# Performance work log

Measured on AMD Instinct MI355X. Metric: run time of the kernel, lower is better.

The kernel has to match this reference:

```python
import jax, jax.numpy as jnp
import numpy as np

B, T, N_EMBD = 4, 2048, 1024
NUM_EXPERTS, TOP_K = 8, 2
N_CITIES = 4
LIN = N_EMBD + 32 + N_EMBD // 4 + N_EMBD // 4 + N_EMBD // 8 + N_EMBD // 8  # 1824


def setup_inputs() -> dict:
    key = jax.random.key(0)
    ks = jax.random.split(key, 12)
    s = 0.02  # init std as in _init_weights
    return {
        "x": jax.random.normal(ks[0], (B, T, N_EMBD), jnp.float32),
        "delta_t_info": jax.random.normal(ks[1], (B, T, N_EMBD // 4), jnp.float32),
        "delta_dis_info": jax.random.normal(ks[2], (B, T, N_EMBD // 4), jnp.float32),
        "delta_rg_info": jax.random.normal(ks[3], (B, T, N_EMBD // 8), jnp.float32),
        "delta_entropy_info": jax.random.normal(ks[4], (B, T, N_EMBD // 8), jnp.float32),
        "city_embeddings": jax.random.normal(ks[5], (N_CITIES, 32), jnp.float32),
        "Wg": jax.random.normal(ks[6], (LIN, NUM_EXPERTS), jnp.float32) * s,
        "bg": jnp.zeros((NUM_EXPERTS,), jnp.float32),
        "W1": jax.random.normal(ks[7], (NUM_EXPERTS, N_EMBD, 4 * N_EMBD), jnp.float32) * s,
        "b1": jnp.zeros((NUM_EXPERTS, 4 * N_EMBD), jnp.float32),
        "W2": jax.random.normal(ks[8], (NUM_EXPERTS, 4 * N_EMBD, N_EMBD), jnp.float32) * s,
        "b2": jnp.zeros((NUM_EXPERTS, N_EMBD), jnp.float32),
        "city_index": 1,
    }


def _moe(x, dt, dd, drg, de, city_embeddings, Wg, bg, W1, b1, W2, b2, city_index):
    b, t, _ = x.shape
    city = jnp.broadcast_to(city_embeddings[city_index], (b, t, 32))
    feats = jnp.concatenate([x, city, dt, dd, drg, de], axis=-1)  # [B,T,LIN]
    logits = jnp.einsum("btl,le->bte", feats, Wg) + bg            # eval mode: no noise
    gate1 = jax.nn.softmax(logits, axis=-1)
    _, topi = jax.lax.top_k(logits, TOP_K)                        # [B,T,k]
    # mask of top-k experts per token; scatter(-inf elsewhere) + softmax
    mask = jax.nn.one_hot(topi, NUM_EXPERTS, dtype=jnp.float32).sum(axis=-2) > 0
    sparse_logits = jnp.where(mask, logits, -jnp.inf)
    gates = jax.nn.softmax(sparse_logits, axis=-1)                # zeros outside top-k
    out = jnp.zeros_like(x)
    for e in range(NUM_EXPERTS):  # fixed small expert set
        h = jax.nn.gelu(jnp.einsum("btc,ch->bth", x, W1[e]) + b1[e], approximate=True)
        y = jnp.einsum("bth,hc->btc", h, W2[e]) + b2[e]
        out = out + gates[..., e:e + 1] * y  # gate is exactly 0 for non-topk tokens
    return out, gate1


def reference(x, delta_t_info, delta_dis_info, delta_rg_info, delta_entropy_info,
              city_embeddings, Wg, bg, W1, b1, W2, b2, city_index):
    return _moe(x, delta_t_info, delta_dis_info, delta_rg_info, delta_entropy_info,
                city_embeddings, Wg, bg, W1, b1, W2, b2, city_index)
```

## Files before the change

### kernel.cpp

```cpp
#include <hip/hip_runtime.h>
#include <hip/hip_bf16.h>
#include <stdint.h>

#define NTOK 8192
#define DEMB 1024
#define HDIM 4096
#define NEXP 8
#define LINF 1824
#define MAXPAD 17280

typedef __attribute__((ext_vector_type(8))) __bf16 bf16x8;
typedef __attribute__((ext_vector_type(4))) __bf16 bf16x4v;
typedef __attribute__((ext_vector_type(4))) float f32x4;

__device__ __forceinline__ void gload_lds16(const void* g, void* l) {
  __builtin_amdgcn_global_load_lds(
      (const __attribute__((address_space(1))) void*)g,
      (__attribute__((address_space(3))) void*)l, 16, 0, 0);
}

__device__ __forceinline__ float dot4(float4 a, float4 b) {
  return a.x*b.x + a.y*b.y + a.z*b.z + a.w*b.w;
}

__global__ void __launch_bounds__(256) k_logits(
    const float* __restrict__ x, const float* __restrict__ dt,
    const float* __restrict__ dd, const float* __restrict__ drg,
    const float* __restrict__ de, const float* __restrict__ city,
    const float* __restrict__ Wg, const float* __restrict__ bg,
    const int* __restrict__ city_index,
    float* __restrict__ gate1, int* __restrict__ top_i, float2* __restrict__ top_g)
{
  __shared__ float WgT[NEXP * LINF];
  const int tid = threadIdx.x;
  const float4* Wg4 = (const float4*)Wg;
  for (int i = tid; i < LINF * NEXP / 4; i += 256) {
    float4 v = Wg4[i];
    int e0 = (i & 1) * 4, f = i >> 1;
    WgT[(e0+0)*LINF + f] = v.x; WgT[(e0+1)*LINF + f] = v.y;
    WgT[(e0+2)*LINF + f] = v.z; WgT[(e0+3)*LINF + f] = v.w;
  }
  __syncthreads();

  const int wave = tid >> 6, lane = tid & 63;
  const int ci = city_index[0];
  const float4* city4 = (const float4*)(city + ci*32);
  const float4 z4 = {0.f, 0.f, 0.f, 0.f};

  #pragma unroll
  for (int k = 0; k < 4; ++k) {
    const int t = blockIdx.x*16 + wave*4 + k;
    const float4* x4 = (const float4*)x + (size_t)t*256;
    float4 xv0 = x4[lane], xv1 = x4[64+lane], xv2 = x4[128+lane], xv3 = x4[192+lane];
    float4 cv = (lane < 8) ? city4[lane] : z4;
    float4 tv = ((const float4*)dt)[(size_t)t*64 + lane];
    float4 dv = ((const float4*)dd)[(size_t)t*64 + lane];
    float4 rv = z4, ev = z4;
    if (lane < 32) {
      rv = ((const float4*)drg)[(size_t)t*32 + lane];
      ev = ((const float4*)de )[(size_t)t*32 + lane];
    }
    float a[8];
    const int l8 = lane & 7, l32 = lane & 31;
    #pragma unroll
    for (int e = 0; e < 8; ++e) {
      const float4* W = (const float4*)(WgT + e*LINF);
      float s = dot4(xv0, W[lane]) + dot4(xv1, W[64+lane])
              + dot4(xv2, W[128+lane]) + dot4(xv3, W[192+lane]);
      s += dot4(cv, W[256 + l8]);
      s += dot4(tv, W[264 + lane]) + dot4(dv, W[328 + lane]);
      s += dot4(rv, W[392 + l32]) + dot4(ev, W[424 + l32]);
      a[e] = s;
    }
    #pragma unroll
    for (int off = 32; off > 0; off >>= 1)
      #pragma unroll
      for (int e = 0; e < 8; ++e) a[e] += __shfl_xor(a[e], off);

    float lg[8];
    #pragma unroll
    for (int e = 0; e < 8; ++e) lg[e] = a[e] + bg[e];
    float mx = lg[0];
    #pragma unroll
    for (int e = 1; e < 8; ++e) mx = fmaxf(mx, lg[e]);
    float ex[8]; float s = 0.f;
    #pragma unroll
    for (int e = 0; e < 8; ++e) { ex[e] = expf(lg[e] - mx); s += ex[e]; }
    int i1 = 0; float l1 = lg[0];
    #pragma unroll
    for (int e = 1; e < 8; ++e) if (lg[e] > l1) { l1 = lg[e]; i1 = e; }
    int i2 = -1; float l2 = -1e30f;
    #pragma unroll
    for (int e = 0; e < 8; ++e) if (e != i1 && lg[e] > l2) { l2 = lg[e]; i2 = e; }
    float e2 = expf(l2 - l1);

    if (lane == 0) {
      float inv = 1.f / s;
      float4 o0 = { ex[0]*inv, ex[1]*inv, ex[2]*inv, ex[3]*inv };
      float4 o1 = { ex[4]*inv, ex[5]*inv, ex[6]*inv, ex[7]*inv };
      float4* gp = (float4*)(gate1 + (size_t)t*8);
      gp[0] = o0; gp[1] = o1;
      top_i[t] = i1 | (i2 << 4);
      float2 g = { 1.f / (1.f + e2), e2 / (1.f + e2) };
      top_g[t] = g;
    }
  }
}

__global__ void __launch_bounds__(256) k_build(
    const int* __restrict__ top_i, const float2* __restrict__ top_g,
    int* __restrict__ counts, int* __restrict__ ex_tok, float* __restrict__ ex_gate,
    int2* __restrict__ ppos)
{
  __shared__ int lcnt[8], lbase[8];
  const int tid = threadIdx.x;
  if (tid < 8) lcnt[tid] = 0;
  __syncthreads();
  const int t = blockIdx.x*256 + tid;
  const int ti = top_i[t];
  const int i1 = ti & 15, i2 = ti >> 4;
  const float2 g = top_g[t];
  int p1 = atomicAdd(&lcnt[i1], 1);
  int p2 = atomicAdd(&lcnt[i2], 1);
  __syncthreads();
  if (tid < 8) lbase[tid] = atomicAdd(&counts[tid], lcnt[tid]);
  __syncthreads();
  int s1 = lbase[i1] + p1; ex_tok[i1*NTOK+s1] = t; ex_gate[i1*NTOK+s1] = g.x;
  int s2 = lbase[i2] + p2; ex_tok[i2*NTOK+s2] = t; ex_gate[i2*NTOK+s2] = g.y;
  int2 pp = { i1 | (s1 << 3), i2 | (s2 << 3) };
  ppos[t] = pp;
}

__global__ void k_finalize(const int* __restrict__ counts, int* __restrict__ seg) {
  if (threadIdx.x == 0 && blockIdx.x == 0) {
    int s = 0;
    for (int e = 0; e < 8; ++e) { seg[e] = s; s += (counts[e] + 127) & ~127; }
    seg[8] = s;
  }
}

__global__ void __launch_bounds__(256) k_conv_x(
    const float4* __restrict__ x, bf16x4v* __restrict__ xb, int n4)
{
  int step = gridDim.x * blockDim.x;
  for (int i = blockIdx.x*blockDim.x + threadIdx.x; i < n4; i += step) {
    float4 v = x[i];
    bf16x4v o;
    o[0] = (__bf16)v.x; o[1] = (__bf16)v.y; o[2] = (__bf16)v.z; o[3] = (__bf16)v.w;
    xb[i] = o;
  }
}

template<int RDIM, int CDIM>
__global__ void __launch_bounds__(256) k_tconv(
    const float* __restrict__ W, __bf16* __restrict__ WT)
{
  const int e  = blockIdx.z;
  const int c0 = blockIdx.x * 64, r0 = blockIdx.y * 64;
  __shared__ float tb[64 * 65];
  const float* src = W  + (size_t)e * RDIM * CDIM + (size_t)r0 * CDIM + c0;
  __bf16*      dst = WT + (size_t)e * RDIM * CDIM + (size_t)c0 * RDIM + r0;
  const int tx = threadIdx.x & 15, ty = threadIdx.x >> 4;
  #pragma unroll
  for (int i = 0; i < 4; ++i) {
    int r = ty + i*16;
    float4 v = *(const float4*)(src + (size_t)r*CDIM + tx*4);
    tb[(tx*4+0)*65 + r] = v.x; tb[(tx*4+1)*65 + r] = v.y;
    tb[(tx*4+2)*65 + r] = v.z; tb[(tx*4+3)*65 + r] = v.w;
  }
  __syncthreads();
  const int seg = threadIdx.x & 7, dr8 = threadIdx.x >> 3;
  #pragma unroll
  for (int i = 0; i < 2; ++i) {
    int d = dr8 + i*32;
    const float* row = tb + d*65 + seg*8;
    bf16x8 o;
    #pragma unroll
    for (int j = 0; j < 8; ++j) o[j] = (__bf16)row[j];
    *(bf16x8*)(dst + (size_t)d*RDIM + seg*8) = o;
  }
}

template<int KDIM, int NDIM, bool G1>
__global__ void __launch_bounds__(512, 2) k_moe_gemm(
    const __bf16* __restrict__ Abase, const __bf16* __restrict__ WT,
    const float* __restrict__ bias,
    const int* __restrict__ seg, const int* __restrict__ counts,
    const int* __restrict__ ex_tok,
    int chunk0, __bf16* __restrict__ dstbuf)
{
  constexpr int NT = KDIM / 64;
  constexpr int BUFB = 49152;

  const int nx = gridDim.x, ny = gridDim.y;
  const int nwg = nx * ny;
  int flat = blockIdx.x + nx * blockIdx.y;
  {
    int q = nwg >> 3, r = nwg & 7;
    int xcd = flat & 7, idx = flat >> 3;
    flat = (xcd < r ? xcd * (q + 1) : r * (q + 1) + (xcd - r) * q) + idx;
  }
  int bx, by;
  if (G1) { bx = flat % nx; by = flat / nx; }
  else    { by = flat % ny; bx = flat / ny; }

  const int segtot = seg[8];
  const int row0 = chunk0 + bx * 128;
  if (row0 >= segtot) return;
  int e = 0;
  #pragma unroll
  for (int qq = 1; qq < 8; ++qq) if (row0 >= seg[qq]) e = qq;
  const int cnt  = counts[e];
  const int sege = seg[e];
  const int n0 = by * 256;

  __shared__ __align__(16) char smem[3 * BUFB];

  const int tid = threadIdx.x;
  const int wid = tid >> 6, lane = tid & 63;
  const int wm = wid >> 2, wn = wid & 3;
  const int l15 = lane & 15, l4 = lane >> 4;
  const __bf16* Bsrc = WT + (size_t)e * NDIM * KDIM;

  const __bf16* asrc[2]; const __bf16* bsrc[4];
  #pragma unroll
  for (int i = 0; i < 2; ++i) {
    int g = i*512 + tid;
    int rr = g >> 3;
    int kb = (g & 7) ^ (rr & 7);
    int arow;
    if (G1) {
      int lr = row0 + rr - sege;
      arow = (lr < cnt) ? ex_tok[e*NTOK + lr] : 0;
    } else {
      arow = row0 + rr - chunk0;
    }
    asrc[i] = Abase + (size_t)arow * KDIM + kb*8;
  }
  #pragma unroll
  for (int i = 0; i < 4; ++i) {
    int g = i*512 + tid;
    int rr = g >> 3;
    int kb = (g & 7) ^ (rr & 7);
    bsrc[i] = Bsrc + (size_t)(n0 + rr) * KDIM + kb*8;
  }

  int aoff[2][4], boff[2][4];
  #pragma unroll
  for (int kk = 0; kk < 2; ++kk) {
    const int kblk = kk*4 + l4;
    const int xo = (kblk ^ (l15 & 7)) * 16;
    #pragma unroll
    for (int m = 0; m < 4; ++m)
      aoff[kk][m] = (wm*64 + m*16 + l15)*128 + xo;
    #pragma unroll
    for (int n = 0; n < 4; ++n)
      boff[kk][n] = 16384 + (wn*64 + n*16 + l15)*128 + xo;
  }

  float bv[4];
  #pragma unroll
  for (int n = 0; n < 4; ++n)
    bv[n] = bias[(size_t)e*NDIM + n0 + wn*64 + n*16 + l15];

  auto STAGE = [&](int t, int b) {
    char* base = smem + b*BUFB;
    #pragma unroll
    for (int i = 0; i < 2; ++i)
      gload_lds16(asrc[i] + t*64, base + (i*512 + tid)*16);
    #pragma unroll
    for (int i = 0; i < 4; ++i)
      gload_lds16(bsrc[i] + t*64, base + 16384 + (i*512 + tid)*16);
  };

  f32x4 acc[4][4] = {};

  STAGE(0, 0);
  STAGE(1, 1);
  asm volatile("s_waitcnt vmcnt(6)" ::: "memory");
  __builtin_amdgcn_s_barrier();
  __builtin_amdgcn_sched_barrier(0);

  int cur = 0;
  for (int t = 0; t < NT; ++t) {
    const char* cb = smem + cur*BUFB;
    int b2 = cur + 2; if (b2 >= 3) b2 -= 3;
    char* sb = smem + b2*BUFB;
    const bool dost = (t + 2 < NT);

    {
      bf16x8 af[4], bfv[4];
      #pragma unroll
      for (int m = 0; m < 4; ++m) af[m]  = *(const bf16x8*)(cb + aoff[0][m]);
      #pragma unroll
      for (int n = 0; n < 4; ++n) bfv[n] = *(const bf16x8*)(cb + boff[0][n]);
      if (dost) {
        gload_lds16(asrc[0] + (t+2)*64, sb + (0*512 + tid)*16);
        gload_lds16(asrc[1] + (t+2)*64, sb + (1*512 + tid)*16);
        gload_lds16(bsrc[0] + (t+2)*64, sb + 16384 + (0*512 + tid)*16);
      }
      __builtin_amdgcn_sched_barrier(0);
      __builtin_amdgcn_s_barrier();
      __builtin_amdgcn_s_setprio(1);
      #pragma unroll
      for (int m = 0; m < 4; ++m)
        #pragma unroll
        for (int n = 0; n < 4; ++n)
          acc[m][n] = __builtin_amdgcn_mfma_f32_16x16x32_bf16(af[m], bfv[n], acc[m][n], 0, 0, 0);
      __builtin_amdgcn_s_setprio(0);
      __builtin_amdgcn_sched_barrier(0);
      __builtin_amdgcn_s_barrier();
    }
    {
      bf16x8 af[4], bfv[4];
      #pragma unroll
      for (int m = 0; m < 4; ++m) af[m]  = *(const bf16x8*)(cb + aoff[1][m]);
      #pragma unroll
      for (int n = 0; n < 4; ++n) bfv[n] = *(const bf16x8*)(cb + boff[1][n]);
      if (dost) {
        gload_lds16(bsrc[1] + (t+2)*64, sb + 16384 + (1*512 + tid)*16);
        gload_lds16(bsrc[2] + (t+2)*64, sb + 16384 + (2*512 + tid)*16);
        gload_lds16(bsrc[3] + (t+2)*64, sb + 16384 + (3*512 + tid)*16);
      }
      __builtin_amdgcn_sched_barrier(0);
      __builtin_amdgcn_s_barrier();
      __builtin_amdgcn_s_setprio(1);
      #pragma unroll
      for (int m = 0; m < 4; ++m)
        #pragma unroll
        for (int n = 0; n < 4; ++n)
          acc[m][n] = __builtin_amdgcn_mfma_f32_16x16x32_bf16(af[m], bfv[n], acc[m][n], 0, 0, 0);
      __builtin_amdgcn_s_setprio(0);
      __builtin_amdgcn_sched_barrier(0);
      asm volatile("s_waitcnt lgkmcnt(0)" ::: "memory");
      if (dost) asm volatile("s_waitcnt vmcnt(6)" ::: "memory");
      else      asm volatile("s_waitcnt vmcnt(0)" ::: "memory");
      __builtin_amdgcn_s_barrier();
      __builtin_amdgcn_sched_barrier(0);
    }
    cur = (cur == 2) ? 0 : cur + 1;
  }

  __bf16* Cl = (__bf16*)smem;
  #pragma unroll
  for (int n = 0; n < 4; ++n) {
    #pragma unroll
    for (int m = 0; m < 4; ++m) {
      #pragma unroll
      for (int r2 = 0; r2 < 4; ++r2) {
        float v = acc[m][n][r2] + bv[n];
        if (G1) {
          float z = 2.302208f * (v + 0.044715f * v * v * v);
          v = v / (1.f + exp2f(-z));
        }
        Cl[(wm*64 + m*16 + l4*4 + r2)*256 + wn*64 + n*16 + l15] = (__bf16)v;
      }
    }
  }
  __syncthreads();
  const int drow0 = G1 ? (row0 - chunk0) : row0;
  #pragma unroll
  for (int it = 0; it < 8; ++it) {
    int idx2 = it*512 + tid;
    int rr = idx2 >> 5, c8 = (idx2 & 31) * 8;
    *(bf16x8*)(dstbuf + (size_t)(drow0 + rr)*NDIM + n0 + c8) =
        *(const bf16x8*)(Cl + rr*256 + c8);
  }
}

__global__ void __launch_bounds__(256) k_combine(
    const __bf16* __restrict__ pbuf, const int2* __restrict__ ppos,
    const float2* __restrict__ top_g, const int* __restrict__ seg,
    float* __restrict__ out)
{
  const int t = blockIdx.x;
  const int tid = threadIdx.x;
  const int2 pp = ppos[t];
  const float2 g = top_g[t];
  const int e1 = pp.x & 7, i1 = pp.x >> 3;
  const int e2 = pp.y & 7, i2 = pp.y >> 3;
  const __bf16* r1 = pbuf + (size_t)(seg[e1] + i1) * DEMB;
  const __bf16* r2 = pbuf + (size_t)(seg[e2] + i2) * DEMB;
  float* orow = out + (size_t)t * DEMB;
  const int c = tid * 4;
  bf16x4v a = *(const bf16x4v*)(r1 + c);
  bf16x4v b = *(const bf16x4v*)(r2 + c);
  float4 o;
  o.x = g.x*(float)a[0] + g.y*(float)b[0];
  o.y = g.x*(float)a[1] + g.y*(float)b[1];
  o.z = g.x*(float)a[2] + g.y*(float)b[2];
  o.w = g.x*(float)a[3] + g.y*(float)b[3];
  *(float4*)(orow + c) = o;
}

extern "C" void kernel_launch(void* const* d_in, const int* in_sizes, int n_in,
                              void* d_out, int out_size, void* d_ws, size_t ws_size,
                              hipStream_t stream)
{
  const float* x   = (const float*)d_in[0];
  const float* dt  = (const float*)d_in[1];
  const float* dd  = (const float*)d_in[2];
  const float* drg = (const float*)d_in[3];
  const float* de  = (const float*)d_in[4];
  const float* city= (const float*)d_in[5];
  const float* Wg  = (const float*)d_in[6];
  const float* bg  = (const float*)d_in[7];
  const float* W1  = (const float*)d_in[8];
  const float* b1  = (const float*)d_in[9];
  const float* W2  = (const float*)d_in[10];
  const float* b2  = (const float*)d_in[11];
  const int* city_index = (const int*)d_in[12];

  float* out   = (float*)d_out;
  float* gate1 = out + (size_t)NTOK * DEMB;

  char* p = (char*)d_ws;
  int*    counts  = (int*)p;      p += 256;
  int*    seg     = (int*)p;      p += 256;
  int*    top_i   = (int*)p;      p += (size_t)NTOK*4;
  float2* top_g   = (float2*)p;   p += (size_t)NTOK*8;
  int2*   ppos    = (int2*)p;     p += (size_t)NTOK*8;
  int*    ex_tok  = (int*)p;      p += (size_t)NTOK*NEXP*4;
  float*  ex_gate = (float*)p;    p += (size_t)NTOK*NEXP*4;
  __bf16* xb      = (__bf16*)p;   p += (size_t)NTOK*DEMB*2;
  __bf16* W1T     = (__bf16*)p;   p += (size_t)NEXP*DEMB*HDIM*2;
  __bf16* W2T     = (__bf16*)p;   p += (size_t)NEXP*DEMB*HDIM*2;
  __bf16* pbuf    = (__bf16*)p;   p += (size_t)MAXPAD*DEMB*2;
  __bf16* hbuf    = (__bf16*)p;

  size_t fixed = (size_t)(p - (char*)d_ws);
  int CH = MAXPAD;
  while (CH > 0 && fixed + (size_t)CH * HDIM * 2 > ws_size) CH -= 256;
  if (CH <= 0) return;
  int nch = (MAXPAD + CH - 1) / CH;

  (void)hipMemsetAsync(counts, 0, 64, stream);

  k_conv_x<<<2048, 256, 0, stream>>>((const float4*)x, (bf16x4v*)xb, NTOK*DEMB/4);
  k_tconv<DEMB, HDIM><<<dim3(HDIM/64, DEMB/64, NEXP), 256, 0, stream>>>(W1, W1T);
  k_tconv<HDIM, DEMB><<<dim3(DEMB/64, HDIM/64, NEXP), 256, 0, stream>>>(W2, W2T);

  k_logits<<<NTOK/16, 256, 0, stream>>>(x, dt, dd, drg, de, city, Wg, bg,
                                        city_index, gate1, top_i, top_g);
  k_build<<<NTOK/256, 256, 0, stream>>>(top_i, top_g, counts, ex_tok, ex_gate, ppos);
  k_finalize<<<1, 64, 0, stream>>>(counts, seg);

  for (int c = 0; c < nch; ++c) {
    k_moe_gemm<DEMB, HDIM, true><<<dim3(CH/128, HDIM/256), 512, 0, stream>>>(
        xb, W1T, b1, seg, counts, ex_tok, c*CH, hbuf);
    k_moe_gemm<HDIM, DEMB, false><<<dim3(CH/128, DEMB/256), 512, 0, stream>>>(
        hbuf, W2T, b2, seg, counts, ex_tok, c*CH, pbuf);
  }
  k_combine<<<NTOK, 256, 0, stream>>>(pbuf, ppos, top_g, seg, out);
}
```

Before: 549.2 us.

## Use 256x256 GEMM tiles with quadrant pipelining and split-K for second GEMM

The expert GEMM tile grows from 128x256 to 256x256 per workgroup. The k-loop becomes a double-buffered four-quadrant schedule that interleaves LDS reads, async global-to-LDS loads and MFMA blocks. Expert segments are now padded to 256 rows to fit the larger tile. The down-projection GEMM is split along K into two halves, each written to its own partial buffer, and the combine kernel sums both partials and adds b2. This is meant to raise arithmetic intensity and cut LDS/global traffic per FLOP, at the cost of more padding rows, an extra partial buffer with more combine reads, and heavier register pressure from 32 accumulators per thread.

```diff
diff --git a/kernel.cpp b/kernel.cpp
--- a/kernel.cpp
+++ b/kernel.cpp
@@ -7,7 +7,7 @@
 #define HDIM 4096
 #define NEXP 8
 #define LINF 1824
-#define MAXPAD 17280
+#define MAXPAD 18432
 
 typedef __attribute__((ext_vector_type(8))) __bf16 bf16x8;
 typedef __attribute__((ext_vector_type(4))) __bf16 bf16x4v;
@@ -134,7 +134,7 @@
 __global__ void k_finalize(const int* __restrict__ counts, int* __restrict__ seg) {
   if (threadIdx.x == 0 && blockIdx.x == 0) {
     int s = 0;
-    for (int e = 0; e < 8; ++e) { seg[e] = s; s += (counts[e] + 127) & ~127; }
+    for (int e = 0; e < 8; ++e) { seg[e] = s; s += (counts[e] + 255) & ~255; }
     seg[8] = s;
   }
 }
@@ -169,20 +169,20 @@
     tb[(tx*4+2)*65 + r] = v.z; tb[(tx*4+3)*65 + r] = v.w;
   }
   __syncthreads();
-  const int seg = threadIdx.x & 7, dr8 = threadIdx.x >> 3;
+  const int sg = threadIdx.x & 7, dr8 = threadIdx.x >> 3;
   #pragma unroll
   for (int i = 0; i < 2; ++i) {
     int d = dr8 + i*32;
-    const float* row = tb + d*65 + seg*8;
+    const float* row = tb + d*65 + sg*8;
     bf16x8 o;
     #pragma unroll
     for (int j = 0; j < 8; ++j) o[j] = (__bf16)row[j];
-    *(bf16x8*)(dst + (size_t)d*RDIM + seg*8) = o;
-  }
-}
-
-template<int KDIM, int NDIM, bool G1>
-__global__ void __launch_bounds__(512, 2) k_moe_gemm(
+    *(bf16x8*)(dst + (size_t)d*RDIM + sg*8) = o;
+  }
+}
+
+template<int KDIM, int KFULL, int NDIM, bool G1>
+__global__ void __launch_bounds__(512, 2) k_moe_gemm8(
     const __bf16* __restrict__ Abase, const __bf16* __restrict__ WT,
     const float* __restrict__ bias,
     const int* __restrict__ seg, const int* __restrict__ counts,
@@ -190,180 +190,214 @@
     int chunk0, __bf16* __restrict__ dstbuf)
 {
   constexpr int NT = KDIM / 64;
-  constexpr int BUFB = 49152;
-
-  const int nx = gridDim.x, ny = gridDim.y;
-  const int nwg = nx * ny;
-  int flat = blockIdx.x + nx * blockIdx.y;
-  {
-    int q = nwg >> 3, r = nwg & 7;
-    int xcd = flat & 7, idx = flat >> 3;
-    flat = (xcd < r ? xcd * (q + 1) : r * (q + 1) + (xcd - r) * q) + idx;
-  }
-  int bx, by;
-  if (G1) { bx = flat % nx; by = flat / nx; }
-  else    { by = flat % ny; bx = flat / ny; }
+  const int nx = gridDim.x, ny = gridDim.y, nz = gridDim.z;
+  const int total = nx * ny * nz;
+  int flat;
+  if (G1) flat = blockIdx.x + nx * blockIdx.y;
+  else    flat = blockIdx.y + ny * (blockIdx.x + nx * blockIdx.z);
+  { int q = total >> 3, r = total & 7; int xcd = flat & 7, idx = flat >> 3;
+    flat = (xcd < r ? xcd*(q+1) : r*(q+1) + (xcd-r)*q) + idx; }
+  int bx, by, bz;
+  if (G1) { bx = flat % nx; by = flat / nx; bz = 0; }
+  else    { by = flat % ny; int f2 = flat / ny; bx = f2 % nx; bz = f2 / nx; }
 
   const int segtot = seg[8];
-  const int row0 = chunk0 + bx * 128;
+  const int row0 = chunk0 + bx * 256;
   if (row0 >= segtot) return;
   int e = 0;
   #pragma unroll
   for (int qq = 1; qq < 8; ++qq) if (row0 >= seg[qq]) e = qq;
-  const int cnt  = counts[e];
-  const int sege = seg[e];
+  const int cnt = counts[e], sege = seg[e];
   const int n0 = by * 256;
-
-  __shared__ __align__(16) char smem[3 * BUFB];
+  const int kbase = bz * KDIM;
+
+  __shared__ __align__(16) char smem[131072];
 
   const int tid = threadIdx.x;
   const int wid = tid >> 6, lane = tid & 63;
   const int wm = wid >> 2, wn = wid & 3;
   const int l15 = lane & 15, l4 = lane >> 4;
-  const __bf16* Bsrc = WT + (size_t)e * NDIM * KDIM;
-
-  const __bf16* asrc[2]; const __bf16* bsrc[4];
-  #pragma unroll
-  for (int i = 0; i < 2; ++i) {
-    int g = i*512 + tid;
-    int rr = g >> 3;
-    int kb = (g & 7) ^ (rr & 7);
-    int arow;
-    if (G1) {
-      int lr = row0 + rr - sege;
-      arow = (lr < cnt) ? ex_tok[e*NTOK + lr] : 0;
-    } else {
-      arow = row0 + rr - chunk0;
-    }
-    asrc[i] = Abase + (size_t)arow * KDIM + kb*8;
-  }
-  #pragma unroll
-  for (int i = 0; i < 4; ++i) {
-    int g = i*512 + tid;
-    int rr = g >> 3;
-    int kb = (g & 7) ^ (rr & 7);
-    bsrc[i] = Bsrc + (size_t)(n0 + rr) * KDIM + kb*8;
-  }
-
-  int aoff[2][4], boff[2][4];
-  #pragma unroll
-  for (int kk = 0; kk < 2; ++kk) {
-    const int kblk = kk*4 + l4;
-    const int xo = (kblk ^ (l15 & 7)) * 16;
-    #pragma unroll
-    for (int m = 0; m < 4; ++m)
-      aoff[kk][m] = (wm*64 + m*16 + l15)*128 + xo;
-    #pragma unroll
-    for (int n = 0; n < 4; ++n)
-      boff[kk][n] = 16384 + (wn*64 + n*16 + l15)*128 + xo;
-  }
+  const __bf16* Bsrc = WT + (size_t)e * NDIM * KFULL;
 
   float bv[4];
-  #pragma unroll
-  for (int n = 0; n < 4; ++n)
-    bv[n] = bias[(size_t)e*NDIM + n0 + wn*64 + n*16 + l15];
-
-  auto STAGE = [&](int t, int b) {
-    char* base = smem + b*BUFB;
-    #pragma unroll
-    for (int i = 0; i < 2; ++i)
-      gload_lds16(asrc[i] + t*64, base + (i*512 + tid)*16);
-    #pragma unroll
-    for (int i = 0; i < 4; ++i)
-      gload_lds16(bsrc[i] + t*64, base + 16384 + (i*512 + tid)*16);
+  if (G1) {
+    #pragma unroll
+    for (int N = 0; N < 4; ++N)
+      bv[N] = bias[(size_t)e*NDIM + n0 + wn*64 + N*16 + l15];
+    asm volatile("" :: "v"(bv[0]), "v"(bv[1]), "v"(bv[2]), "v"(bv[3]));
+  }
+
+  const __bf16* sp[4][2];
+  #pragma unroll
+  for (int j = 0; j < 2; ++j) {
+    int g = j*512 + tid;
+    int sl = g >> 3;
+    int kb = (g & 7) ^ (sl & 7);
+    #pragma unroll
+    for (int mh = 0; mh < 2; ++mh) {
+      int wms = (sl >> 6) & 1, rs = sl & 63;
+      int R = wms*128 + mh*64 + rs;
+      int arow;
+      if (G1) { int lr = row0 + R - sege; arow = (lr < cnt) ? ex_tok[e*NTOK + lr] : 0; }
+      else    { arow = row0 + R - chunk0; }
+      sp[mh][j] = Abase + (size_t)arow * KFULL + kbase + kb*8;
+    }
+    #pragma unroll
+    for (int nh = 0; nh < 2; ++nh) {
+      int wns = (sl >> 5) & 3, rs = sl & 31;
+      int C = wns*64 + nh*32 + rs;
+      sp[2+nh][j] = Bsrc + (size_t)(n0 + C) * KFULL + kbase + kb*8;
+    }
+  }
+
+  int xo[2];
+  #pragma unroll
+  for (int kk = 0; kk < 2; ++kk) xo[kk] = (((kk*4 + l4) ^ (l15 & 7)) * 16);
+  int arb[4], brb[2];
+  #pragma unroll
+  for (int m = 0; m < 4; ++m) arb[m] = (wm*64 + m*16 + l15) * 128;
+  #pragma unroll
+  for (int n = 0; n < 2; ++n) brb[n] = 32768 + (wn*32 + n*16 + l15) * 128;
+
+  auto ISSUE = [&](int h, int tt) {
+    char* b = smem + (tt & 1) * 65536 + h * 16384;
+    gload_lds16(sp[h][0] + tt*64, b + tid*16);
+    gload_lds16(sp[h][1] + tt*64, b + 8192 + tid*16);
   };
 
-  f32x4 acc[4][4] = {};
-
-  STAGE(0, 0);
-  STAGE(1, 1);
-  asm volatile("s_waitcnt vmcnt(6)" ::: "memory");
+  f32x4 acc[8][4] = {};
+
+  ISSUE(0,0); ISSUE(2,0); ISSUE(3,0); ISSUE(1,0); ISSUE(0,1);
+  asm volatile("s_waitcnt vmcnt(2)" ::: "memory");
   __builtin_amdgcn_s_barrier();
   __builtin_amdgcn_sched_barrier(0);
 
-  int cur = 0;
   for (int t = 0; t < NT; ++t) {
-    const char* cb = smem + cur*BUFB;
-    int b2 = cur + 2; if (b2 >= 3) b2 -= 3;
-    char* sb = smem + b2*BUFB;
-    const bool dost = (t + 2 < NT);
-
-    {
-      bf16x8 af[4], bfv[4];
-      #pragma unroll
-      for (int m = 0; m < 4; ++m) af[m]  = *(const bf16x8*)(cb + aoff[0][m]);
-      #pragma unroll
-      for (int n = 0; n < 4; ++n) bfv[n] = *(const bf16x8*)(cb + boff[0][n]);
-      if (dost) {
-        gload_lds16(asrc[0] + (t+2)*64, sb + (0*512 + tid)*16);
-        gload_lds16(asrc[1] + (t+2)*64, sb + (1*512 + tid)*16);
-        gload_lds16(bsrc[0] + (t+2)*64, sb + 16384 + (0*512 + tid)*16);
-      }
-      __builtin_amdgcn_sched_barrier(0);
-      __builtin_amdgcn_s_barrier();
-      __builtin_amdgcn_s_setprio(1);
-      #pragma unroll
-      for (int m = 0; m < 4; ++m)
+    const char* cb = smem + (t & 1) * 65536;
+    const bool last = (t == NT - 1);
+    bf16x8 af[4][2], bfr[2][2][2];
+
+    #pragma unroll
+    for (int m = 0; m < 4; ++m)
+      #pragma unroll
+      for (int kk = 0; kk < 2; ++kk)
+        af[m][kk] = *(const bf16x8*)(cb + arb[m] + xo[kk]);
+    #pragma unroll
+    for (int n = 0; n < 2; ++n)
+      #pragma unroll
+      for (int kk = 0; kk < 2; ++kk)
+        bfr[0][n][kk] = *(const bf16x8*)(cb + brb[n] + xo[kk]);
+    if (!last) ISSUE(2, t+1);
+    __builtin_amdgcn_sched_barrier(0);
+    __builtin_amdgcn_s_barrier();
+    __builtin_amdgcn_sched_barrier(0);
+    __builtin_amdgcn_s_setprio(1);
+    #pragma unroll
+    for (int m = 0; m < 4; ++m)
+      #pragma unroll
+      for (int n = 0; n < 2; ++n)
         #pragma unroll
-        for (int n = 0; n < 4; ++n)
-          acc[m][n] = __builtin_amdgcn_mfma_f32_16x16x32_bf16(af[m], bfv[n], acc[m][n], 0, 0, 0);
-      __builtin_amdgcn_s_setprio(0);
-      __builtin_amdgcn_sched_barrier(0);
-      __builtin_amdgcn_s_barrier();
-    }
-    {
-      bf16x8 af[4], bfv[4];
-      #pragma unroll
-      for (int m = 0; m < 4; ++m) af[m]  = *(const bf16x8*)(cb + aoff[1][m]);
-      #pragma unroll
-      for (int n = 0; n < 4; ++n) bfv[n] = *(const bf16x8*)(cb + boff[1][n]);
-      if (dost) {
-        gload_lds16(bsrc[1] + (t+2)*64, sb + 16384 + (1*512 + tid)*16);
-        gload_lds16(bsrc[2] + (t+2)*64, sb + 16384 + (2*512 + tid)*16);
-        gload_lds16(bsrc[3] + (t+2)*64, sb + 16384 + (3*512 + tid)*16);
-      }
-      __builtin_amdgcn_sched_barrier(0);
-      __builtin_amdgcn_s_barrier();
-      __builtin_amdgcn_s_setprio(1);
-      #pragma unroll
-      for (int m = 0; m < 4; ++m)
+        for (int kk = 0; kk < 2; ++kk)
+          acc[m][n] = __builtin_amdgcn_mfma_f32_16x16x32_bf16(af[m][kk], bfr[0][n][kk], acc[m][n], 0, 0, 0);
+    __builtin_amdgcn_s_setprio(0);
+    __builtin_amdgcn_sched_barrier(0);
+    if (!last) asm volatile("s_waitcnt vmcnt(6)" ::: "memory");
+    else       asm volatile("s_waitcnt vmcnt(2)" ::: "memory");
+    __builtin_amdgcn_s_barrier();
+    __builtin_amdgcn_sched_barrier(0);
+
+    #pragma unroll
+    for (int n = 0; n < 2; ++n)
+      #pragma unroll
+      for (int kk = 0; kk < 2; ++kk)
+        bfr[1][n][kk] = *(const bf16x8*)(cb + 16384 + brb[n] + xo[kk]);
+    if (!last) ISSUE(3, t+1);
+    __builtin_amdgcn_sched_barrier(0);
+    __builtin_amdgcn_s_barrier();
+    __builtin_amdgcn_sched_barrier(0);
+    __builtin_amdgcn_s_setprio(1);
+    #pragma unroll
+    for (int m = 0; m < 4; ++m)
+      #pragma unroll
+      for (int n = 0; n < 2; ++n)
         #pragma unroll
-        for (int n = 0; n < 4; ++n)
-          acc[m][n] = __builtin_amdgcn_mfma_f32_16x16x32_bf16(af[m], bfv[n], acc[m][n], 0, 0, 0);
-      __builtin_amdgcn_s_setprio(0);
-      __builtin_amdgcn_sched_barrier(0);
-      asm volatile("s_waitcnt lgkmcnt(0)" ::: "memory");
-      if (dost) asm volatile("s_waitcnt vmcnt(6)" ::: "memory");
-      else      asm volatile("s_waitcnt vmcnt(0)" ::: "memory");
-      __builtin_amdgcn_s_barrier();
-      __builtin_amdgcn_sched_barrier(0);
-    }
-    cur = (cur == 2) ? 0 : cur + 1;
-  }
-
+        for (int kk = 0; kk < 2; ++kk)
+          acc[m][2+n] = __builtin_amdgcn_mfma_f32_16x16x32_bf16(af[m][kk], bfr[1][n][kk], acc[m][2+n], 0, 0, 0);
+    __builtin_amdgcn_s_setprio(0);
+    __builtin_amdgcn_sched_barrier(0);
+    if (!last) asm volatile("s_waitcnt vmcnt(6)" ::: "memory");
+    else       asm volatile("s_waitcnt vmcnt(0)" ::: "memory");
+    __builtin_amdgcn_s_barrier();
+    __builtin_amdgcn_sched_barrier(0);
+
+    #pragma unroll
+    for (int m = 0; m < 4; ++m)
+      #pragma unroll
+      for (int kk = 0; kk < 2; ++kk)
+        af[m][kk] = *(const bf16x8*)(cb + 16384 + arb[m] + xo[kk]);
+    if (!last) ISSUE(1, t+1);
+    __builtin_amdgcn_sched_barrier(0);
+    __builtin_amdgcn_s_barrier();
+    __builtin_amdgcn_sched_barrier(0);
+    __builtin_amdgcn_s_setprio(1);
+    #pragma unroll
+    for (int m = 0; m < 4; ++m)
+      #pragma unroll
+      for (int n = 0; n < 2; ++n)
+        #pragma unroll
+        for (int kk = 0; kk < 2; ++kk)
+          acc[4+m][n] = __builtin_amdgcn_mfma_f32_16x16x32_bf16(af[m][kk], bfr[0][n][kk], acc[4+m][n], 0, 0, 0);
+    __builtin_amdgcn_s_setprio(0);
+    __builtin_amdgcn_sched_barrier(0);
+    __builtin_amdgcn_s_barrier();
+    __builtin_amdgcn_sched_barrier(0);
+
+    if (t + 2 < NT) ISSUE(0, t+2);
+    __builtin_amdgcn_sched_barrier(0);
+    __builtin_amdgcn_s_barrier();
+    __builtin_amdgcn_sched_barrier(0);
+    __builtin_amdgcn_s_setprio(1);
+    #pragma unroll
+    for (int m = 0; m < 4; ++m)
+      #pragma unroll
+      for (int n = 0; n < 2; ++n)
+        #pragma unroll
+        for (int kk = 0; kk < 2; ++kk)
+          acc[4+m][2+n] = __builtin_amdgcn_mfma_f32_16x16x32_bf16(af[m][kk], bfr[1][n][kk], acc[4+m][2+n], 0, 0, 0);
+    __builtin_amdgcn_s_setprio(0);
+    __builtin_amdgcn_sched_barrier(0);
+    if (t + 1 < NT - 1)      asm volatile("s_waitcnt vmcnt(6)" ::: "memory");
+    else if (t + 1 == NT - 1) asm volatile("s_waitcnt vmcnt(4)" ::: "memory");
+    __builtin_amdgcn_s_barrier();
+    __builtin_amdgcn_sched_barrier(0);
+  }
+
+  __syncthreads();
   __bf16* Cl = (__bf16*)smem;
   #pragma unroll
-  for (int n = 0; n < 4; ++n) {
-    #pragma unroll
-    for (int m = 0; m < 4; ++m) {
+  for (int M = 0; M < 8; ++M) {
+    #pragma unroll
+    for (int N = 0; N < 4; ++N) {
       #pragma unroll
       for (int r2 = 0; r2 < 4; ++r2) {
-        float v = acc[m][n][r2] + bv[n];
+        float v = acc[M][N][r2];
         if (G1) {
+          v += bv[N];
           float z = 2.302208f * (v + 0.044715f * v * v * v);
           v = v / (1.f + exp2f(-z));
         }
-        Cl[(wm*64 + m*16 + l4*4 + r2)*256 + wn*64 + n*16 + l15] = (__bf16)v;
+        Cl[(wm*128 + M*16 + l4*4 + r2)*256 + wn*64 + N*16 + l15] = (__bf16)v;
       }
     }
   }
   __syncthreads();
   const int drow0 = G1 ? (row0 - chunk0) : row0;
-  #pragma unroll
-  for (int it = 0; it < 8; ++it) {
+  __bf16* dst = dstbuf + (G1 ? (size_t)0 : (size_t)bz * MAXPAD * NDIM);
+  #pragma unroll
+  for (int it = 0; it < 16; ++it) {
     int idx2 = it*512 + tid;
     int rr = idx2 >> 5, c8 = (idx2 & 31) * 8;
-    *(bf16x8*)(dstbuf + (size_t)(drow0 + rr)*NDIM + n0 + c8) =
+    *(bf16x8*)(dst + (size_t)(drow0 + rr)*NDIM + n0 + c8) =
         *(const bf16x8*)(Cl + rr*256 + c8);
   }
 }
@@ -371,26 +405,30 @@
 __global__ void __launch_bounds__(256) k_combine(
     const __bf16* __restrict__ pbuf, const int2* __restrict__ ppos,
     const float2* __restrict__ top_g, const int* __restrict__ seg,
-    float* __restrict__ out)
-{
-  const int t = blockIdx.x;
-  const int tid = threadIdx.x;
+    const float* __restrict__ b2, float* __restrict__ out)
+{
+  const int t = blockIdx.x, tid = threadIdx.x;
   const int2 pp = ppos[t];
   const float2 g = top_g[t];
   const int e1 = pp.x & 7, i1 = pp.x >> 3;
   const int e2 = pp.y & 7, i2 = pp.y >> 3;
-  const __bf16* r1 = pbuf + (size_t)(seg[e1] + i1) * DEMB;
-  const __bf16* r2 = pbuf + (size_t)(seg[e2] + i2) * DEMB;
-  float* orow = out + (size_t)t * DEMB;
+  const size_t r1 = (size_t)(seg[e1] + i1) * DEMB;
+  const size_t r2 = (size_t)(seg[e2] + i2) * DEMB;
+  const __bf16* p0 = pbuf;
+  const __bf16* p1 = pbuf + (size_t)MAXPAD * DEMB;
   const int c = tid * 4;
-  bf16x4v a = *(const bf16x4v*)(r1 + c);
-  bf16x4v b = *(const bf16x4v*)(r2 + c);
+  bf16x4v a0 = *(const bf16x4v*)(p0 + r1 + c);
+  bf16x4v a1 = *(const bf16x4v*)(p1 + r1 + c);
+  bf16x4v c0 = *(const bf16x4v*)(p0 + r2 + c);
+  bf16x4v c1 = *(const bf16x4v*)(p1 + r2 + c);
+  float4 ba = *(const float4*)(b2 + (size_t)e1*DEMB + c);
+  float4 bb = *(const float4*)(b2 + (size_t)e2*DEMB + c);
   float4 o;
-  o.x = g.x*(float)a[0] + g.y*(float)b[0];
-  o.y = g.x*(float)a[1] + g.y*(float)b[1];
-  o.z = g.x*(float)a[2] + g.y*(float)b[2];
-  o.w = g.x*(float)a[3] + g.y*(float)b[3];
-  *(float4*)(orow + c) = o;
+  o.x = g.x*((float)a0[0]+(float)a1[0]+ba.x) + g.y*((float)c0[0]+(float)c1[0]+bb.x);
+  o.y = g.x*((float)a0[1]+(float)a1[1]+ba.y) + g.y*((float)c0[1]+(float)c1[1]+bb.y);
+  o.z = g.x*((float)a0[2]+(float)a1[2]+ba.z) + g.y*((float)c0[2]+(float)c1[2]+bb.z);
+  o.w = g.x*((float)a0[3]+(float)a1[3]+ba.w) + g.y*((float)c0[3]+(float)c1[3]+bb.w);
+  *(float4*)(out + (size_t)t*DEMB + c) = o;
 }
 
 extern "C" void kernel_launch(void* const* d_in, const int* in_sizes, int n_in,
@@ -425,7 +463,7 @@
   __bf16* xb      = (__bf16*)p;   p += (size_t)NTOK*DEMB*2;
   __bf16* W1T     = (__bf16*)p;   p += (size_t)NEXP*DEMB*HDIM*2;
   __bf16* W2T     = (__bf16*)p;   p += (size_t)NEXP*DEMB*HDIM*2;
-  __bf16* pbuf    = (__bf16*)p;   p += (size_t)MAXPAD*DEMB*2;
+  __bf16* pbuf    = (__bf16*)p;   p += (size_t)2*MAXPAD*DEMB*2;
   __bf16* hbuf    = (__bf16*)p;
 
   size_t fixed = (size_t)(p - (char*)d_ws);
@@ -446,10 +484,10 @@
   k_finalize<<<1, 64, 0, stream>>>(counts, seg);
 
   for (int c = 0; c < nch; ++c) {
-    k_moe_gemm<DEMB, HDIM, true><<<dim3(CH/128, HDIM/256), 512, 0, stream>>>(
+    k_moe_gemm8<1024, 1024, HDIM, true><<<dim3(CH/256, HDIM/256, 1), 512, 0, stream>>>(
         xb, W1T, b1, seg, counts, ex_tok, c*CH, hbuf);
-    k_moe_gemm<HDIM, DEMB, false><<<dim3(CH/128, DEMB/256), 512, 0, stream>>>(
+    k_moe_gemm8<2048, 4096, DEMB, false><<<dim3(CH/256, DEMB/256, 2), 512, 0, stream>>>(
         hbuf, W2T, b2, seg, counts, ex_tok, c*CH, pbuf);
   }
-  k_combine<<<NTOK, 256, 0, stream>>>(pbuf, ppos, top_g, seg, out);
-}
+  k_combine<<<NTOK, 256, 0, stream>>>(pbuf, ppos, top_g, seg, b2, out);
+}
```

Result: faster. 525.0 us (-4.4%).
